# Kernel tuning notes

Hardware: AMD Instinct MI355X
Metric: run time of the kernel (lower is better)

The kernel has to match this reference:

```python
import jax, jax.numpy as jnp
import numpy as np
import math

B, N = 1, 512
C_S, C_Z, C_H, H = 384, 128, 16, 12
P_Q, P_V, NBINS = 4, 8, 64
OUT_DIM = H * (C_H + P_V * 4 + C_Z)


def setup_inputs() -> dict:
    key = jax.random.key(0)
    ks = jax.random.split(key, 16)
    def rn(k, shape, scale=1.0):
        return jax.random.normal(k, shape, dtype=jnp.float32) * scale
    rotations, _ = jnp.linalg.qr(rn(ks[3], (B, N, 3, 3)))  # orthogonal frames
    w = 0.02
    return {
        "s": rn(ks[0], (B, N, C_S)),
        "z": rn(ks[1], (B, N, N, C_Z)),
        "translations": rn(ks[2], (B, N, 3), 10.0),  # spread over ~0-32 A bins
        "rotations": rotations,
        "Wq": rn(ks[4], (C_S, H * C_H), w), "bq": jnp.zeros((H * C_H,), jnp.float32),
        "Wk": rn(ks[5], (C_S, H * C_H), w), "bk": jnp.zeros((H * C_H,), jnp.float32),
        "Wv": rn(ks[6], (C_S, H * C_H), w), "bv": jnp.zeros((H * C_H,), jnp.float32),
        "Wqp": rn(ks[7], (C_S, H * P_Q * 3), w), "bqp": jnp.zeros((H * P_Q * 3,), jnp.float32),
        "Wkp": rn(ks[8], (C_S, H * P_Q * 3), w), "bkp": jnp.zeros((H * P_Q * 3,), jnp.float32),
        "Wvp": rn(ks[9], (C_S, H * P_V * 3), w), "bvp": jnp.zeros((H * P_V * 3,), jnp.float32),
        "Wb": rn(ks[10], (C_Z, H), w), "bb": jnp.zeros((H,), jnp.float32),
        "emb": rn(ks[11], (NBINS, H), w),
        "scale_logits": jnp.zeros((3, H), jnp.float32),
        "head_weights": jnp.ones((H,), jnp.float32),
        "Wout": rn(ks[12], (OUT_DIM, C_S), w), "bout": jnp.zeros((C_S,), jnp.float32),
    }


def reference(s, z, translations, rotations, Wq, bq, Wk, bk, Wv, bv, Wqp, bqp, Wkp, bkp, Wvp, bvp, Wb, bb, emb, scale_logits, head_weights, Wout, bout):
    b, n, _ = s.shape
    t = translations
    q = (s @ Wq + bq).reshape(b, n, H, C_H)
    k = (s @ Wk + bk).reshape(b, n, H, C_H)
    v = (s @ Wv + bv).reshape(b, n, H, C_H)
    q_pts = (s @ Wqp + bqp).reshape(b, n, H, P_Q, 3)
    k_pts = (s @ Wkp + bkp).reshape(b, n, H, P_Q, 3)
    v_pts = (s @ Wvp + bvp).reshape(b, n, H, P_V, 3)
    # local -> global frame
    q_g = jnp.einsum('bnij,bnhpj->bnhpi', rotations, q_pts) + t[:, :, None, None, :]
    k_g = jnp.einsum('bnij,bnhpj->bnhpi', rotations, k_pts) + t[:, :, None, None, :]
    v_g = jnp.einsum('bnij,bnhpj->bnhpi', rotations, v_pts) + t[:, :, None, None, :]
    scalar_logits = jnp.einsum('bnhc,bmhc->bnmh', q, k) / math.sqrt(C_H)  # [b,n,m,h]
    point_dist = jnp.sum((q_g[:, :, None] - k_g[:, None]) ** 2, axis=-1)  # [b,n,m,h,p]
    point_logits = -0.5 * jnp.sum(point_dist, axis=-1) * head_weights[None, None, None, :]
    pair_bias = z @ Wb + bb  # [b,n,m,h]
    pair_dist = jnp.linalg.norm(t[:, :, None, :] - t[:, None, :, :], axis=-1)  # [b,n,m]
    edges = jnp.linspace(0.0, 32.0, NBINS + 1)
    bins = jnp.clip(jnp.searchsorted(edges, pair_dist, side='left') - 1, 0, NBINS - 1)
    dist_bias = emb[bins]  # [b,n,m,h]
    scales = jnp.stack([
        (pair_dist <= 5.0).astype(s.dtype),
        ((pair_dist > 5.0) & (pair_dist <= 15.0)).astype(s.dtype),
        jnp.ones_like(pair_dist),
    ], axis=-1)  # [b,n,m,3]
    per_head = jax.nn.softmax(scale_logits, axis=0)  # [3,h]
    multiscale = jnp.einsum('bnms,sh->bnmh', scales, per_head)
    logits = scalar_logits + point_logits + pair_bias + dist_bias + multiscale
    attn = jax.nn.softmax(logits.astype(jnp.float32), axis=2).astype(s.dtype)  # over m
    out_scalar = jnp.einsum('bnmh,bmhc->bnhc', attn, v)
    out_pts_g = jnp.einsum('bnmh,bmhpi->bnhpi', attn, v_g)
    # global -> local frame (R^T applied)
    out_pts_l = jnp.einsum('bnji,bnhpj->bnhpi', rotations, out_pts_g - t[:, :, None, None, :])
    out_norms = jnp.linalg.norm(out_pts_l, axis=-1)  # [b,n,h,p]
    pair_feat = jnp.einsum('bnmh,bnmc->bnhc', attn, z)
    feats = jnp.concatenate([
        out_scalar,
        out_pts_l.reshape(b, n, H, P_V * 3),
        out_norms,
        pair_feat,
    ], axis=-1).reshape(b, n, -1)  # [b,n,OUT_DIM]
    return feats @ Wout + bout
```

## Files before the change

kernel.cpp:

```cpp
#include <hip/hip_runtime.h>

#define NTOK 512
#define CS 384
#define CZ 128
#define CH 16
#define HN 12
#define PQ 4
#define PV 8
#define FEAT_DIM 2112
#define HSEG 176

__global__ __launch_bounds__(256) void k_proj(
    const float* __restrict__ s,
    const float* __restrict__ Wq,  const float* __restrict__ bq,
    const float* __restrict__ Wk,  const float* __restrict__ bk,
    const float* __restrict__ Wv,  const float* __restrict__ bv,
    const float* __restrict__ Wqp, const float* __restrict__ bqp,
    const float* __restrict__ Wkp, const float* __restrict__ bkp,
    const float* __restrict__ Wvp, const float* __restrict__ bvp,
    float* __restrict__ qs, float* __restrict__ ksT, float* __restrict__ vs,
    float* __restrict__ raw_g)
{
    __shared__ float s_l[16 * CS];
    __shared__ float Ws[16][64];
    const int t  = threadIdx.x;
    const int n0 = blockIdx.x * 16;

    const float4* sg  = (const float4*)(s + (size_t)n0 * CS);
    float4*       sl4 = (float4*)s_l;
#pragma unroll
    for (int j = 0; j < 6; ++j) sl4[j * 256 + t] = sg[j * 256 + t];

    const int col = blockIdx.y * 64 + (t & 63);
    const int tq  = t >> 6;
    const float* bv_;
    int lc;
    if (col < 192)      { bv_ = bq;  lc = col;       }
    else if (col < 384) { bv_ = bk;  lc = col - 192; }
    else if (col < 576) { bv_ = bv;  lc = col - 384; }
    else if (col < 720) { bv_ = bqp; lc = col - 576; }
    else if (col < 864) { bv_ = bkp; lc = col - 720; }
    else                { bv_ = bvp; lc = col - 864; }

    const int kk_s = t >> 4, cq = t & 15;
    const int gcol = blockIdx.y * 64 + cq * 4;
    const float* Wsrc; int lcs, ncs;
    if (gcol < 192)      { Wsrc = Wq;  lcs = gcol;       ncs = 192; }
    else if (gcol < 384) { Wsrc = Wk;  lcs = gcol - 192; ncs = 192; }
    else if (gcol < 576) { Wsrc = Wv;  lcs = gcol - 384; ncs = 192; }
    else if (gcol < 720) { Wsrc = Wqp; lcs = gcol - 576; ncs = 144; }
    else if (gcol < 864) { Wsrc = Wkp; lcs = gcol - 720; ncs = 144; }
    else                 { Wsrc = Wvp; lcs = gcol - 864; ncs = 288; }

    float a0, a1, a2, a3;
    a0 = a1 = a2 = a3 = bv_[lc];
    __syncthreads();

    for (int ks = 0; ks < CS; ks += 16) {
        float4 w4 = *(const float4*)&Wsrc[(size_t)(ks + kk_s) * ncs + lcs];
        __syncthreads();
        *(float4*)&Ws[kk_s][cq * 4] = w4;
        __syncthreads();
        const float* srow = s_l + tq * 4 * CS + ks;
#pragma unroll
        for (int kk = 0; kk < 16; ++kk) {
            float w = Ws[kk][t & 63];
            a0 += srow[kk] * w;
            a1 += srow[CS + kk] * w;
            a2 += srow[2 * CS + kk] * w;
            a3 += srow[3 * CS + kk] * w;
        }
    }

    const int n = n0 + tq * 4;
    if (col < 192) {
        qs[(size_t)(n + 0) * 192 + lc] = a0;
        qs[(size_t)(n + 1) * 192 + lc] = a1;
        qs[(size_t)(n + 2) * 192 + lc] = a2;
        qs[(size_t)(n + 3) * 192 + lc] = a3;
    } else if (col < 384) {
        float* p = ksT + (size_t)lc * NTOK + n;
        p[0] = a0; p[1] = a1; p[2] = a2; p[3] = a3;
    } else if (col < 576) {
        vs[(size_t)(n + 0) * 192 + lc] = a0;
        vs[(size_t)(n + 1) * 192 + lc] = a1;
        vs[(size_t)(n + 2) * 192 + lc] = a2;
        vs[(size_t)(n + 3) * 192 + lc] = a3;
    } else {
        const int pc = col - 576;
        raw_g[(size_t)(n + 0) * 576 + pc] = a0;
        raw_g[(size_t)(n + 1) * 576 + pc] = a1;
        raw_g[(size_t)(n + 2) * 576 + pc] = a2;
        raw_g[(size_t)(n + 3) * 576 + pc] = a3;
    }
}

__global__ __launch_bounds__(256) void k_frame(
    const float* __restrict__ raw_g,
    const float* __restrict__ trans,
    const float* __restrict__ rot,
    float* __restrict__ qg, float* __restrict__ kgT, float* __restrict__ vg,
    float* __restrict__ transT)
{
    const int e = blockIdx.x * 256 + threadIdx.x;
    if (e < 512 * 576) {
        const int n = e / 576, loc = e % 576;
        const int i = loc % 3, base = loc - i;
        const float* rp = raw_g + (size_t)n * 576 + base;
        float x0 = rp[0], x1 = rp[1], x2 = rp[2];
        const float* R = rot + (size_t)n * 9 + i * 3;
        float v = trans[(size_t)n * 3 + i] + R[0] * x0 + R[1] * x1 + R[2] * x2;
        if (loc < 144)      qg[(size_t)n * 144 + loc] = v;
        else if (loc < 288) kgT[(size_t)(loc - 144) * NTOK + n] = v;
        else                vg[(size_t)n * 288 + loc - 288] = v;
    } else {
        const int idx = e - 512 * 576;
        if (idx < 3 * NTOK) {
            const int m = idx / 3, i = idx % 3;
            transT[(size_t)i * NTOK + m] = trans[(size_t)m * 3 + i];
        }
    }
}

__global__ __launch_bounds__(256, 2) void k_mid(
    const float* __restrict__ z,
    const float* __restrict__ qs, const float* __restrict__ ksT,
    const float* __restrict__ qg, const float* __restrict__ kgT,
    const float* __restrict__ trans, const float* __restrict__ transT,
    const float* __restrict__ Wb, const float* __restrict__ bbv,
    const float* __restrict__ emb, const float* __restrict__ slog,
    const float* __restrict__ hw,
    float* __restrict__ attn, float* __restrict__ feats)
{
    __shared__ __align__(16) float lgT[NTOK * HN];
    __shared__ __align__(16) float zl[64 * 132];
    __shared__ __align__(16) float wbT[HN * CZ];
    __shared__ float embl[64 * HN];
    __shared__ float ql[192];
    __shared__ float qgl[144];
    __shared__ float tl[3];
    __shared__ float phl[36];
    __shared__ float hwl[HN];

    const int n = blockIdx.x, t = threadIdx.x;

    for (int i = t; i < CZ * HN; i += 256) {
        const int h = i >> 7, c = i & 127;
        wbT[h * CZ + c] = Wb[(size_t)c * HN + h];
    }
    for (int i = t; i < 64 * HN; i += 256) embl[i] = emb[i];
    if (t < 192) ql[t] = qs[(size_t)n * 192 + t];
    if (t < 144) qgl[t] = qg[(size_t)n * 144 + t];
    if (t < 3)   tl[t] = trans[(size_t)n * 3 + t];
    if (t < HN)  hwl[t] = hw[t];
    if (t >= 64 && t < 64 + HN) {
        const int h = t - 64;
        float s0 = slog[h], s1 = slog[HN + h], s2 = slog[2 * HN + h];
        float mx = fmaxf(s0, fmaxf(s1, s2));
        float e0 = expf(s0 - mx), e1 = expf(s1 - mx), e2 = expf(s2 - mx);
        float inv = 1.f / (e0 + e1 + e2);
        phl[h] = e0 * inv; phl[12 + h] = e1 * inv; phl[24 + h] = e2 * inv;
    }

    const int ml = t & 63, hg = t >> 6, h0 = hg * 3;
    const float bb0 = bbv[h0], bb1 = bbv[h0 + 1], bb2 = bbv[h0 + 2];

    float4 pf[8];
    {
        const float4* zg = (const float4*)(z + (size_t)n * NTOK * CZ);
#pragma unroll
        for (int j = 0; j < 8; ++j) pf[j] = zg[j * 256 + t];
    }
    __syncthreads();

    const float* w0 = wbT + (h0 + 0) * CZ;
    const float* w1 = wbT + (h0 + 1) * CZ;
    const float* w2 = wbT + (h0 + 2) * CZ;

    for (int mc = 0; mc < 8; ++mc) {
#pragma unroll
        for (int j = 0; j < 8; ++j) {
            const int f = j * 256 + t;
            const int row = f >> 5, c4 = (f & 31) * 4;
            *(float4*)&zl[row * 132 + c4] = pf[j];
        }
        if (mc < 7) {
            const float4* zg = (const float4*)(z + ((size_t)n * NTOK + (mc + 1) * 64) * CZ);
#pragma unroll
            for (int j = 0; j < 8; ++j) pf[j] = zg[j * 256 + t];
        }
        __syncthreads();

        const int mg = mc * 64 + ml;
        float b0 = bb0, b1 = bb1, b2 = bb2;
        const float* zrow = zl + ml * 132;
#pragma unroll 4
        for (int cq = 0; cq < CZ; cq += 4) {
            float4 zv = *(const float4*)&zrow[cq];
            float4 v0 = *(const float4*)&w0[cq];
            float4 v1 = *(const float4*)&w1[cq];
            float4 v2 = *(const float4*)&w2[cq];
            b0 += zv.x * v0.x + zv.y * v0.y + zv.z * v0.z + zv.w * v0.w;
            b1 += zv.x * v1.x + zv.y * v1.y + zv.z * v1.z + zv.w * v1.w;
            b2 += zv.x * v2.x + zv.y * v2.y + zv.z * v2.z + zv.w * v2.w;
        }
        float dx = tl[0] - transT[mg];
        float dy = tl[1] - transT[NTOK + mg];
        float dz = tl[2] - transT[2 * NTOK + mg];
        float dist = sqrtf(dx * dx + dy * dy + dz * dz);
        int bin = min(63, max(0, (int)ceilf(dist * 2.f) - 1));
        const float in5  = (dist <= 5.f) ? 1.f : 0.f;
        const float in15 = (dist > 5.f && dist <= 15.f) ? 1.f : 0.f;

        float acc[3] = {b0, b1, b2};
#pragma unroll
        for (int k = 0; k < 3; ++k) {
            const int h = h0 + k;
            float sc = 0.f;
            const float* kk = ksT + (size_t)h * CH * NTOK + mg;
            const float* qq = ql + h * CH;
#pragma unroll
            for (int c = 0; c < CH; ++c) sc += qq[c] * kk[(size_t)c * NTOK];
            float sd = 0.f;
            const float* kg = kgT + (size_t)h * 12 * NTOK + mg;
            const float* qp = qgl + h * 12;
#pragma unroll
            for (int i = 0; i < 12; ++i) {
                float d = qp[i] - kg[(size_t)i * NTOK];
                sd += d * d;
            }
            acc[k] += sc * 0.25f - 0.5f * sd * hwl[h]
                    + embl[bin * HN + h]
                    + phl[24 + h] + in5 * phl[h] + in15 * phl[12 + h];
        }
        lgT[mg * HN + h0 + 0] = acc[0];
        lgT[mg * HN + h0 + 1] = acc[1];
        lgT[mg * HN + h0 + 2] = acc[2];
        __syncthreads();
    }

    const int lane = t & 63;
#pragma unroll
    for (int hh = 0; hh < 3; ++hh) {
        const int h = h0 + hh;
        float v[8];
        float mx = -1e30f;
#pragma unroll
        for (int i = 0; i < 8; ++i) {
            v[i] = lgT[(lane + 64 * i) * HN + h];
            mx = fmaxf(mx, v[i]);
        }
#pragma unroll
        for (int off = 32; off; off >>= 1) mx = fmaxf(mx, __shfl_xor(mx, off));
        float sm = 0.f;
#pragma unroll
        for (int i = 0; i < 8; ++i) { v[i] = expf(v[i] - mx); sm += v[i]; }
#pragma unroll
        for (int off = 32; off; off >>= 1) sm += __shfl_xor(sm, off);
        const float inv = 1.f / sm;
        float* arow = attn + ((size_t)n * HN + h) * NTOK;
#pragma unroll
        for (int i = 0; i < 8; ++i) {
            float a = v[i] * inv;
            lgT[(lane + 64 * i) * HN + h] = a;
            arow[lane + 64 * i] = a;
        }
    }
    __syncthreads();

    const int slab = t >> 6;
    const int c2 = (t & 63) * 2;
    float pacc[HN][2];
#pragma unroll
    for (int h = 0; h < HN; ++h) { pacc[h][0] = 0.f; pacc[h][1] = 0.f; }
    const float* zp = z + (size_t)n * NTOK * CZ + (size_t)slab * 128 * CZ + c2;
    const float* lp = lgT + slab * 128 * HN;
#pragma unroll 4
    for (int m = 0; m < 128; ++m) {
        float2 zv = *(const float2*)(zp + (size_t)m * CZ);
        float4 a0 = *(const float4*)&lp[m * HN + 0];
        float4 a1 = *(const float4*)&lp[m * HN + 4];
        float4 a2 = *(const float4*)&lp[m * HN + 8];
        pacc[0][0]  += a0.x * zv.x;  pacc[0][1]  += a0.x * zv.y;
        pacc[1][0]  += a0.y * zv.x;  pacc[1][1]  += a0.y * zv.y;
        pacc[2][0]  += a0.z * zv.x;  pacc[2][1]  += a0.z * zv.y;
        pacc[3][0]  += a0.w * zv.x;  pacc[3][1]  += a0.w * zv.y;
        pacc[4][0]  += a1.x * zv.x;  pacc[4][1]  += a1.x * zv.y;
        pacc[5][0]  += a1.y * zv.x;  pacc[5][1]  += a1.y * zv.y;
        pacc[6][0]  += a1.z * zv.x;  pacc[6][1]  += a1.z * zv.y;
        pacc[7][0]  += a1.w * zv.x;  pacc[7][1]  += a1.w * zv.y;
        pacc[8][0]  += a2.x * zv.x;  pacc[8][1]  += a2.x * zv.y;
        pacc[9][0]  += a2.y * zv.x;  pacc[9][1]  += a2.y * zv.y;
        pacc[10][0] += a2.z * zv.x;  pacc[10][1] += a2.z * zv.y;
        pacc[11][0] += a2.w * zv.x;  pacc[11][1] += a2.w * zv.y;
    }
    float* out_l = zl;
    for (int s = 0; s < 4; ++s) {
        __syncthreads();
        if (slab == s) {
#pragma unroll
            for (int h = 0; h < HN; ++h) {
                float* p = &out_l[h * CZ + c2];
                if (s == 0) { p[0] = pacc[h][0]; p[1] = pacc[h][1]; }
                else        { p[0] += pacc[h][0]; p[1] += pacc[h][1]; }
            }
        }
    }
    __syncthreads();
    for (int i = t; i < HN * CZ; i += 256) {
        const int h = i >> 7, c = i & 127;
        feats[(size_t)n * FEAT_DIM + h * HSEG + 48 + c] = out_l[i];
    }
}

__global__ __launch_bounds__(256) void k_outmm(
    const float* __restrict__ attn,
    const float* __restrict__ vs, const float* __restrict__ vg,
    const float* __restrict__ trans,
    const float* __restrict__ rot,
    float* __restrict__ feats)
{
    __shared__ float As_t[64][33];
    __shared__ float Vs[64][40];
    __shared__ float out_l[32 * 40];
    __shared__ float Rl[32][9];
    __shared__ float tl[32][3];
    const int t   = threadIdx.x;
    const int gn0 = blockIdx.x * 32;
    const int h   = blockIdx.y;

    const int slab  = t >> 6;
    const int w     = t & 63;
    const int n0l   = (w >> 3) * 4;
    const int j0    = (w & 7) * 5;

    float acc[4][5];
#pragma unroll
    for (int i = 0; i < 4; ++i)
#pragma unroll
        for (int k = 0; k < 5; ++k) acc[i][k] = 0.f;

    for (int step = 0; step < 8; ++step) {
        const int mb = step * 64;
        __syncthreads();
#pragma unroll
        for (int jj = 0; jj < 2; ++jj) {
            const int f = t + jj * 256;
            const int n_loc = f >> 4, c4 = f & 15;
            float4 a = *(const float4*)&attn[(((size_t)(gn0 + n_loc)) * HN + h) * NTOK + mb + c4 * 4];
            As_t[c4 * 4 + 0][n_loc] = a.x;
            As_t[c4 * 4 + 1][n_loc] = a.y;
            As_t[c4 * 4 + 2][n_loc] = a.z;
            As_t[c4 * 4 + 3][n_loc] = a.w;
        }
#pragma unroll
        for (int jj = 0; jj < 10; ++jj) {
            const int f = t + jj * 256;
            const int m_loc = f / 40, jv = f % 40;
            float v;
            if (jv < 16) v = vs[(size_t)(mb + m_loc) * 192 + h * 16 + jv];
            else         v = vg[(size_t)(mb + m_loc) * 288 + h * 24 + (jv - 16)];
            Vs[m_loc][jv] = v;
        }
        __syncthreads();
#pragma unroll
        for (int mi = 0; mi < 16; ++mi) {
            const int m = slab * 16 + mi;
            float4 a = *(const float4*)&As_t[m][n0l];
            float vv[5];
#pragma unroll
            for (int k = 0; k < 5; ++k) vv[k] = Vs[m][j0 + k];
            const float av[4] = {a.x, a.y, a.z, a.w};
#pragma unroll
            for (int i = 0; i < 4; ++i)
#pragma unroll
                for (int k = 0; k < 5; ++k)
                    acc[i][k] += av[i] * vv[k];
        }
    }

    for (int s = 0; s < 4; ++s) {
        __syncthreads();
        if (slab == s) {
#pragma unroll
            for (int i = 0; i < 4; ++i)
#pragma unroll
                for (int k = 0; k < 5; ++k) {
                    float* p = &out_l[(n0l + i) * 40 + j0 + k];
                    if (s == 0) *p = acc[i][k];
                    else        *p += acc[i][k];
                }
        }
    }
    for (int i = t; i < 32 * 12; i += 256) {
        const int n_loc = i / 12, r = i % 12;
        if (r < 9) Rl[n_loc][r] = rot[(size_t)(gn0 + n_loc) * 9 + r];
        else       tl[n_loc][r - 9] = trans[(size_t)(gn0 + n_loc) * 3 + (r - 9)];
    }
    __syncthreads();

    for (int f = t; f < 32 * 48; f += 256) {
        const int n_loc = f / 48, j = f % 48;
        const float* sh = &out_l[n_loc * 40];
        float* fp = feats + (size_t)(gn0 + n_loc) * FEAT_DIM + h * HSEG;
        const float* R = Rl[n_loc];
        const float* tv = tl[n_loc];
        if (j < 16) {
            fp[j] = sh[j];
        } else if (j < 40) {
            const int jj = j - 16, p = jj / 3, i = jj % 3;
            float val = 0.f;
#pragma unroll
            for (int q = 0; q < 3; ++q) val += R[q * 3 + i] * (sh[16 + p * 3 + q] - tv[q]);
            fp[16 + jj] = val;
        } else {
            const int p = j - 40;
            float s2 = 0.f;
#pragma unroll
            for (int i = 0; i < 3; ++i) {
                float val = 0.f;
#pragma unroll
                for (int q = 0; q < 3; ++q) val += R[q * 3 + i] * (sh[16 + p * 3 + q] - tv[q]);
                s2 += val * val;
            }
            fp[40 + p] = sqrtf(s2);
        }
    }
}

#define KT 16
__global__ __launch_bounds__(256) void k_outproj(
    const float* __restrict__ feats,
    const float* __restrict__ Wout,
    const float* __restrict__ bout,
    float* __restrict__ out)
{
    __shared__ float As[KT][64];
    __shared__ float Bs[KT][64];
    const int t  = threadIdx.x;
    const int n0 = blockIdx.x * 64;
    const int j0 = blockIdx.y * 64;
    const int k0 = blockIdx.z * HSEG;

    const int arow = t >> 2, akq = (t & 3) * 4;
    const int bkk  = t >> 4, bjq = (t & 15) * 4;
    const int tr   = t >> 4, tc  = t & 15;

    float acc[4][4] = {{0.f}};
    for (int s = 0; s < 11; ++s) {
        const int ks = k0 + s * KT;
        float4 a4 = *(const float4*)&feats[(size_t)(n0 + arow) * FEAT_DIM + ks + akq];
        float4 b4 = *(const float4*)&Wout[(size_t)(ks + bkk) * 384 + j0 + bjq];
        __syncthreads();
        As[akq + 0][arow] = a4.x;
        As[akq + 1][arow] = a4.y;
        As[akq + 2][arow] = a4.z;
        As[akq + 3][arow] = a4.w;
        *(float4*)&Bs[bkk][bjq] = b4;
        __syncthreads();
#pragma unroll
        for (int kk = 0; kk < KT; ++kk) {
            float4 av = *(const float4*)&As[kk][tr * 4];
            float4 bv = *(const float4*)&Bs[kk][tc * 4];
            acc[0][0] += av.x * bv.x; acc[0][1] += av.x * bv.y;
            acc[0][2] += av.x * bv.z; acc[0][3] += av.x * bv.w;
            acc[1][0] += av.y * bv.x; acc[1][1] += av.y * bv.y;
            acc[1][2] += av.y * bv.z; acc[1][3] += av.y * bv.w;
            acc[2][0] += av.z * bv.x; acc[2][1] += av.z * bv.y;
            acc[2][2] += av.z * bv.z; acc[2][3] += av.z * bv.w;
            acc[3][0] += av.w * bv.x; acc[3][1] += av.w * bv.y;
            acc[3][2] += av.w * bv.z; acc[3][3] += av.w * bv.w;
        }
    }

    const bool addb = (blockIdx.z == 0);
#pragma unroll
    for (int i = 0; i < 4; ++i) {
        const int row = n0 + tr * 4 + i;
#pragma unroll
        for (int jj = 0; jj < 4; ++jj) {
            const int col = j0 + tc * 4 + jj;
            float v = acc[i][jj];
            if (addb) v += bout[col];
            atomicAdd(&out[(size_t)row * 384 + col], v);
        }
    }
}

extern "C" void kernel_launch(void* const* d_in, const int* in_sizes, int n_in,
                              void* d_out, int out_size, void* d_ws, size_t ws_size,
                              hipStream_t stream) {
    const float* s     = (const float*)d_in[0];
    const float* z     = (const float*)d_in[1];
    const float* trans = (const float*)d_in[2];
    const float* rot   = (const float*)d_in[3];
    const float* Wq    = (const float*)d_in[4];
    const float* bq    = (const float*)d_in[5];
    const float* Wk    = (const float*)d_in[6];
    const float* bk    = (const float*)d_in[7];
    const float* Wv    = (const float*)d_in[8];
    const float* bv    = (const float*)d_in[9];
    const float* Wqp   = (const float*)d_in[10];
    const float* bqp   = (const float*)d_in[11];
    const float* Wkp   = (const float*)d_in[12];
    const float* bkp   = (const float*)d_in[13];
    const float* Wvp   = (const float*)d_in[14];
    const float* bvp   = (const float*)d_in[15];
    const float* Wb    = (const float*)d_in[16];
    const float* bb    = (const float*)d_in[17];
    const float* emb   = (const float*)d_in[18];
    const float* slog  = (const float*)d_in[19];
    const float* hw    = (const float*)d_in[20];
    const float* Wout  = (const float*)d_in[21];
    const float* bout  = (const float*)d_in[22];

    float* W = (float*)d_ws;
    float* qs     = W;
    float* ksT    = qs + 98304;
    float* vs     = ksT + 98304;
    float* qg     = vs + 98304;
    float* kgT    = qg + 73728;
    float* vg     = kgT + 73728;
    float* transT = vg + 147456;
    float* attn   = transT + 1536;
    float* feats  = attn + 3145728;
    float* raw_g  = feats + 1081344;

    k_proj<<<dim3(32, 18), 256, 0, stream>>>(s, Wq, bq, Wk, bk, Wv, bv,
                                             Wqp, bqp, Wkp, bkp, Wvp, bvp,
                                             qs, ksT, vs, raw_g);
    k_frame<<<1158, 256, 0, stream>>>(raw_g, trans, rot, qg, kgT, vg, transT);
    k_mid<<<512, 256, 0, stream>>>(z, qs, ksT, qg, kgT, trans, transT,
                                   Wb, bb, emb, slog, hw, attn, feats);
    k_outmm<<<dim3(16, 12), 256, 0, stream>>>(attn, vs, vg, trans, rot, feats);
    hipMemsetAsync(d_out, 0, (size_t)NTOK * 384 * sizeof(float), stream);
    k_outproj<<<dim3(8, 6, 12), 256, 0, stream>>>(feats, Wout, bout, (float*)d_out);
}
```

Baseline: 412.8 us.

## Double-buffer z chunks via direct global-to-LDS loads with XOR swizzle

Replaces the register-prefetch-then-store staging of z tiles in k_mid with asynchronous global_load_lds copies into a double-buffered, XOR-swizzled shared buffer. Logits are kept in registers instead of a large shared array, and the freed shared memory is reused for the attention and output scratch. This is meant to cut register pressure and LDS footprint, avoid bank conflicts without padding, and overlap loads with compute. The risk is that no explicit wait on the async LDS loads is visible before the buffer is read, so correctness depends on the barrier and the compiler inserting vmcnt waits.

```diff
diff --git a/kernel.cpp b/kernel.cpp
--- a/kernel.cpp
+++ b/kernel.cpp
@@ -122,6 +122,24 @@
     }
 }
 
+__device__ __forceinline__ void stage_chunk(const float* zbase,
+                                            float (*dst)[CZ],
+                                            int mc, int wv, int lane)
+{
+    const int r2 = lane >> 5;
+    const int s0 = lane & 31;
+#pragma unroll
+    for (int j = 0; j < 8; ++j) {
+        const int rl = wv * 16 + 2 * j + r2;
+        const int sl = s0 ^ (rl & 31);
+        const float* gp = zbase + ((size_t)(mc * 64 + rl) * CZ + sl * 4);
+        __builtin_amdgcn_global_load_lds(
+            (const __attribute__((address_space(1))) void*)gp,
+            (__attribute__((address_space(3))) void*)&dst[wv * 16 + 2 * j][0],
+            16, 0, 0);
+    }
+}
+
 __global__ __launch_bounds__(256, 2) void k_mid(
     const float* __restrict__ z,
     const float* __restrict__ qs, const float* __restrict__ ksT,
@@ -132,8 +150,7 @@
     const float* __restrict__ hw,
     float* __restrict__ attn, float* __restrict__ feats)
 {
-    __shared__ __align__(16) float lgT[NTOK * HN];
-    __shared__ __align__(16) float zl[64 * 132];
+    __shared__ __align__(16) float zl[2][64][CZ];
     __shared__ __align__(16) float wbT[HN * CZ];
     __shared__ float embl[64 * HN];
     __shared__ float ql[192];
@@ -143,6 +160,10 @@
     __shared__ float hwl[HN];
 
     const int n = blockIdx.x, t = threadIdx.x;
+    const int lane = t & 63, wv = t >> 6, h0 = wv * 3;
+    const float* zbase = z + (size_t)n * NTOK * CZ;
+
+    stage_chunk(zbase, zl[0], 0, wv, lane);
 
     for (int i = t; i < CZ * HN; i += 256) {
         const int h = i >> 7, c = i & 127;
@@ -162,44 +183,30 @@
         phl[h] = e0 * inv; phl[12 + h] = e1 * inv; phl[24 + h] = e2 * inv;
     }
 
-    const int ml = t & 63, hg = t >> 6, h0 = hg * 3;
     const float bb0 = bbv[h0], bb1 = bbv[h0 + 1], bb2 = bbv[h0 + 2];
 
-    float4 pf[8];
-    {
-        const float4* zg = (const float4*)(z + (size_t)n * NTOK * CZ);
-#pragma unroll
-        for (int j = 0; j < 8; ++j) pf[j] = zg[j * 256 + t];
-    }
     __syncthreads();
 
     const float* w0 = wbT + (h0 + 0) * CZ;
     const float* w1 = wbT + (h0 + 1) * CZ;
     const float* w2 = wbT + (h0 + 2) * CZ;
-
+    const int rx = lane & 31;
+
+    float lgr[3][8];
+
+#pragma unroll
     for (int mc = 0; mc < 8; ++mc) {
-#pragma unroll
-        for (int j = 0; j < 8; ++j) {
-            const int f = j * 256 + t;
-            const int row = f >> 5, c4 = (f & 31) * 4;
-            *(float4*)&zl[row * 132 + c4] = pf[j];
-        }
-        if (mc < 7) {
-            const float4* zg = (const float4*)(z + ((size_t)n * NTOK + (mc + 1) * 64) * CZ);
-#pragma unroll
-            for (int j = 0; j < 8; ++j) pf[j] = zg[j * 256 + t];
-        }
-        __syncthreads();
-
-        const int mg = mc * 64 + ml;
+        if (mc < 7) stage_chunk(zbase, zl[(mc & 1) ^ 1], mc + 1, wv, lane);
+
+        const int mg = mc * 64 + lane;
         float b0 = bb0, b1 = bb1, b2 = bb2;
-        const float* zrow = zl + ml * 132;
+        const float* zrow = &zl[mc & 1][lane][0];
 #pragma unroll 4
-        for (int cq = 0; cq < CZ; cq += 4) {
-            float4 zv = *(const float4*)&zrow[cq];
-            float4 v0 = *(const float4*)&w0[cq];
-            float4 v1 = *(const float4*)&w1[cq];
-            float4 v2 = *(const float4*)&w2[cq];
+        for (int cq = 0; cq < 32; ++cq) {
+            float4 zv = *(const float4*)&zrow[(cq ^ rx) * 4];
+            float4 v0 = *(const float4*)&w0[cq * 4];
+            float4 v1 = *(const float4*)&w1[cq * 4];
+            float4 v2 = *(const float4*)&w2[cq * 4];
             b0 += zv.x * v0.x + zv.y * v0.y + zv.z * v0.z + zv.w * v0.w;
             b1 += zv.x * v1.x + zv.y * v1.y + zv.z * v1.z + zv.w * v1.w;
             b2 += zv.x * v2.x + zv.y * v2.y + zv.z * v2.z + zv.w * v2.w;
@@ -233,28 +240,26 @@
                     + embl[bin * HN + h]
                     + phl[24 + h] + in5 * phl[h] + in15 * phl[12 + h];
         }
-        lgT[mg * HN + h0 + 0] = acc[0];
-        lgT[mg * HN + h0 + 1] = acc[1];
-        lgT[mg * HN + h0 + 2] = acc[2];
-        __syncthreads();
-    }
-
-    const int lane = t & 63;
+        lgr[0][mc] = acc[0];
+        lgr[1][mc] = acc[1];
+        lgr[2][mc] = acc[2];
+        __syncthreads();
+    }
+
+    float* attn_l = &zl[0][0][0];
+    float* out_l  = &zl[1][0][0];
 #pragma unroll
     for (int hh = 0; hh < 3; ++hh) {
         const int h = h0 + hh;
+        float mx = lgr[hh][0];
+#pragma unroll
+        for (int i = 1; i < 8; ++i) mx = fmaxf(mx, lgr[hh][i]);
+#pragma unroll
+        for (int off = 32; off; off >>= 1) mx = fmaxf(mx, __shfl_xor(mx, off));
         float v[8];
-        float mx = -1e30f;
-#pragma unroll
-        for (int i = 0; i < 8; ++i) {
-            v[i] = lgT[(lane + 64 * i) * HN + h];
-            mx = fmaxf(mx, v[i]);
-        }
-#pragma unroll
-        for (int off = 32; off; off >>= 1) mx = fmaxf(mx, __shfl_xor(mx, off));
         float sm = 0.f;
 #pragma unroll
-        for (int i = 0; i < 8; ++i) { v[i] = expf(v[i] - mx); sm += v[i]; }
+        for (int i = 0; i < 8; ++i) { v[i] = expf(lgr[hh][i] - mx); sm += v[i]; }
 #pragma unroll
         for (int off = 32; off; off >>= 1) sm += __shfl_xor(sm, off);
         const float inv = 1.f / sm;
@@ -262,19 +267,19 @@
 #pragma unroll
         for (int i = 0; i < 8; ++i) {
             float a = v[i] * inv;
-            lgT[(lane + 64 * i) * HN + h] = a;
-            arow[lane + 64 * i] = a;
+            arow[i * 64 + lane] = a;
+            attn_l[(i * 64 + lane) * HN + h] = a;
         }
     }
     __syncthreads();
 
-    const int slab = t >> 6;
-    const int c2 = (t & 63) * 2;
+    const int slab = wv;
+    const int c2 = lane * 2;
     float pacc[HN][2];
 #pragma unroll
     for (int h = 0; h < HN; ++h) { pacc[h][0] = 0.f; pacc[h][1] = 0.f; }
     const float* zp = z + (size_t)n * NTOK * CZ + (size_t)slab * 128 * CZ + c2;
-    const float* lp = lgT + slab * 128 * HN;
+    const float* lp = attn_l + slab * 128 * HN;
 #pragma unroll 4
     for (int m = 0; m < 128; ++m) {
         float2 zv = *(const float2*)(zp + (size_t)m * CZ);
@@ -294,7 +299,6 @@
         pacc[10][0] += a2.z * zv.x;  pacc[10][1] += a2.z * zv.y;
         pacc[11][0] += a2.w * zv.x;  pacc[11][1] += a2.w * zv.y;
     }
-    float* out_l = zl;
     for (int s = 0; s < 4; ++s) {
         __syncthreads();
         if (slab == s) {
```

Result: slower. 901.7 us (+118.4%).
